# Optimization experiments

Measured on AMD Instinct MI355X. Metric: run time of the kernel, lower is better.

The kernel has to match this reference:

```python
import jax, jax.numpy as jnp
import numpy as np

N = 1_000_000      # occupied input voxels
NREF = 400_000     # occupied reference (target) voxels on the stride-2 grid
CIN = 32
COUT = 64
G = 256            # input spatial grid extent per axis
B = 4              # batch size (ME batch index in coords[:, 0])
PRIME = 2654435761 # odd -> bijective multiplier mod 2^26


def _decode_np(ids, g):
    z = ids % g; ids = ids // g
    y = ids % g; ids = ids // g
    x = ids % g; b = ids // g
    return np.stack([b, x, y, z], axis=1).astype(np.int32)


def setup_inputs() -> dict:
    key = jax.random.key(0)
    k1, k2, k3 = jax.random.split(key, 3)
    # unique input voxel coordinates on a B x G^3 grid (bijection mod 2^26)
    ids_in = (np.arange(N, dtype=np.int64) * PRIME) % (B * G ** 3)
    coords = _decode_np(ids_in, G)                      # [N,4] (b,x,y,z), unique
    # unique reference coordinates on the stride-2 output grid
    gh = G // 2
    ids_ref = (np.arange(NREF, dtype=np.int64) * PRIME) % (B * gh ** 3)
    ref = _decode_np(ids_ref, gh)
    ref[:, 1:] *= 2                                     # ME tensor-stride-2 coords
    feats = jax.random.normal(k1, (N, CIN), jnp.float32)
    W = jax.random.normal(k2, (8, CIN, COUT), jnp.float32) * (1.0 / np.sqrt(8 * CIN))
    b = jax.random.normal(k3, (COUT,), jnp.float32) * 0.01
    return {"feats": feats, "W": W, "b": b,
            "coords": jnp.asarray(coords), "ref_coords": jnp.asarray(ref)}


def _ravel(c, step):
    # faithful to get_target_by_sp_tensor: batch-major ravel of 4 columns
    return c[:, 3] + c[:, 2] * step + c[:, 1] * step * step + c[:, 0] * step * step * step


def reference(feats, W, b, coords, ref_coords):
    n = coords.shape[0]
    # --- hash table of input voxels (sorted keys + permuted features) ---
    in_key = ((coords[:, 0] * G + coords[:, 1]) * G + coords[:, 2]) * G + coords[:, 3]
    order = jnp.argsort(in_key)
    skeys = in_key[order]
    sfeats = feats[order]
    # --- output coordinates: stride-2 downsample (kernel=2, stride=2) ---
    p = coords.at[:, 1:].set((coords[:, 1:] // 2) * 2)
    pkey = ((p[:, 0] * G + p[:, 1]) * G + p[:, 2]) * G + p[:, 3]
    out_key = jnp.unique(pkey, size=n, fill_value=-1)   # sorted, padded with -1
    valid = out_key >= 0
    ok = jnp.where(valid, out_key, 0)
    oz = ok % G; r = ok // G
    oy = r % G; r = r // G
    ox = r % G; ob = r // G
    out_coords = jnp.where(valid[:, None], jnp.stack([ob, ox, oy, oz], axis=1), -1)
    # --- sparse conv: gather the 2x2x2 children of each output voxel ---
    acc = jnp.zeros((n, W.shape[2]), feats.dtype)
    offsets = [(dx, dy, dz) for dx in (0, 1) for dy in (0, 1) for dz in (0, 1)]
    for i, (dx, dy, dz) in enumerate(offsets):
        ckey = out_key + dx * G * G + dy * G + dz
        idx = jnp.clip(jnp.searchsorted(skeys, ckey), 0, n - 1)
        found = (skeys[idx] == ckey) & valid
        f = jnp.where(found[:, None], sfeats[idx], 0.0)
        acc = acc + f @ W[i]
    out_feats = jnp.where(valid[:, None], acc + b, 0.0)
    # --- pruning mask: ravel + isin, faithful to get_target_by_sp_tensor ---
    step = jnp.maximum(out_coords.max(), ref_coords.max()).astype(jnp.int32) + 1
    min_value = jnp.minimum(out_coords.min(), ref_coords.min())
    shift = jnp.where(min_value < 0, -min_value, 0)
    oc = out_coords.at[:, 1:].add(shift)
    rc = ref_coords.at[:, 1:].add(shift)
    out1d = _ravel(oc, step)
    ref1d = _ravel(rc, step)
    sref = jnp.sort(ref1d)
    j = jnp.clip(jnp.searchsorted(sref, out1d), 0, sref.shape[0] - 1)
    mask = (sref[j] == out1d) & valid
    out_feats = jnp.where(mask[:, None], out_feats, 0.0)
    return out_coords, out_feats, mask
```

## Files before the change

### kernel.cpp

```cpp
#include <hip/hip_runtime.h>

#define WORDS_P  (1u << 18)
#define NBLK2    1024

typedef float f4_native __attribute__((ext_vector_type(4)));

__device__ __forceinline__ unsigned k23_of(int b, int x, int y, int z) {
  return ((unsigned)b << 21) | ((unsigned)(x >> 1) << 14) |
         ((unsigned)(y >> 1) << 7) | (unsigned)(z >> 1);
}

__device__ __forceinline__ void fill_slice(f4_native* __restrict__ of, size_t lo,
                                           size_t hi, unsigned tid, unsigned nthr) {
  f4_native z = {0.f, 0.f, 0.f, 0.f};
  for (size_t i = lo + tid; i < hi; i += nthr)
    __builtin_nontemporal_store(z, &of[i]);
}

__global__ __launch_bounds__(256) void fill_ws(f4_native* __restrict__ wsz, size_t n4) {
  size_t stride = (size_t)gridDim.x * 256u;
  f4_native z = {0.f, 0.f, 0.f, 0.f};
  for (size_t i = (size_t)blockIdx.x * 256u + threadIdx.x; i < n4; i += stride)
    wsz[i] = z;
}

__global__ __launch_bounds__(256) void build_fill(const int4* __restrict__ coords, int n,
                                                  const int4* __restrict__ ref, int nref,
                                                  unsigned* __restrict__ parbm,
                                                  unsigned* __restrict__ refbm,
                                                  f4_native* __restrict__ ofm,
                                                  size_t lo, size_t hi) {
  unsigned tid = blockIdx.x * 256u + threadIdx.x;
  unsigned nthr = gridDim.x * 256u;
  for (unsigned i = tid; i < (unsigned)(n + nref); i += nthr) {
    if (i < (unsigned)n) {
      int4 c = coords[i];
      unsigned k = k23_of(c.x, c.y, c.z, c.w);
      atomicOr(&parbm[k >> 5], 1u << (k & 31));
    } else {
      int4 c = ref[i - (unsigned)n];
      unsigned k = k23_of(c.x, c.y, c.z, c.w);
      atomicOr(&refbm[k >> 5], 1u << (k & 31));
    }
  }
  fill_slice(ofm, lo, hi, tid, nthr);
}

__global__ __launch_bounds__(256) void pop2(const unsigned* __restrict__ parbm,
                                            unsigned* __restrict__ refbm,
                                            unsigned* __restrict__ bsums,
                                            f4_native* __restrict__ ofm,
                                            size_t lo, size_t hi) {
  __shared__ unsigned s[256];
  unsigned t = threadIdx.x;
  unsigned w = blockIdx.x * 256u + t;
  unsigned p = parbm[w];
  unsigned m = p & refbm[w];
  refbm[w] = m;
  s[t] = __popc(p); __syncthreads();
  for (int off = 128; off > 0; off >>= 1) { if (t < (unsigned)off) s[t] += s[t + off]; __syncthreads(); }
  if (t == 0) bsums[blockIdx.x] = s[0];
  __syncthreads();
  s[t] = __popc(m); __syncthreads();
  for (int off = 128; off > 0; off >>= 1) { if (t < (unsigned)off) s[t] += s[t + off]; __syncthreads(); }
  if (t == 0) bsums[NBLK2 + blockIdx.x] = s[0];

  fill_slice(ofm, lo, hi, blockIdx.x * 256u + t, gridDim.x * 256u);
}

__global__ __launch_bounds__(256) void prefix2b(const unsigned* __restrict__ parbm,
                                                const unsigned* __restrict__ maskbm,
                                                const unsigned* __restrict__ bsums,
                                                unsigned* __restrict__ parpre,
                                                unsigned* __restrict__ maskpre,
                                                unsigned* __restrict__ clist,
                                                unsigned* __restrict__ counter,
                                                f4_native* __restrict__ ofm,
                                                size_t lo, size_t hi) {
  __shared__ unsigned s[256];
  __shared__ unsigned basP_s, basM_s;
  unsigned t = threadIdx.x, blk = blockIdx.x;
  unsigned accP = 0, accM = 0;
  for (unsigned idx = t; idx < blk; idx += 256u) {
    accP += bsums[idx];
    accM += bsums[NBLK2 + idx];
  }
  s[t] = accP; __syncthreads();
  for (int off = 128; off > 0; off >>= 1) { if (t < (unsigned)off) s[t] += s[t + off]; __syncthreads(); }
  if (t == 0) basP_s = s[0];
  __syncthreads();
  s[t] = accM; __syncthreads();
  for (int off = 128; off > 0; off >>= 1) { if (t < (unsigned)off) s[t] += s[t + off]; __syncthreads(); }
  if (t == 0) basM_s = s[0];
  __syncthreads();
  unsigned basP = basP_s, basM = basM_s;

  unsigned w = blk * 256u + t;
  unsigned pw = parbm[w], mw = maskbm[w];
  unsigned cp = __popc(pw), cm = __popc(mw);
  s[t] = cp; __syncthreads();
  for (int off = 1; off < 256; off <<= 1) {
    unsigned v = (t >= (unsigned)off) ? s[t - off] : 0u;
    __syncthreads(); s[t] += v; __syncthreads();
  }
  unsigned ppre = basP + ((t == 0) ? 0u : s[t - 1]);
  parpre[w] = ppre;
  unsigned plast = basP + s[255];
  __syncthreads();
  s[t] = cm; __syncthreads();
  for (int off = 1; off < 256; off <<= 1) {
    unsigned v = (t >= (unsigned)off) ? s[t - off] : 0u;
    __syncthreads(); s[t] += v; __syncthreads();
  }
  unsigned mpre = basM + ((t == 0) ? 0u : s[t - 1]);
  maskpre[w] = mpre;
  for (unsigned k = 0; k < cm * 8u; k++) clist[mpre * 8u + k] = 0u;
  if (blk == NBLK2 - 1u && t == 255u) {
    counter[0] = basM + s[255];
    counter[1] = plast;
  }

  fill_slice(ofm, lo, hi, blk * 256u + t, gridDim.x * 256u);
}

__global__ __launch_bounds__(256) void scatter_emit(const int4* __restrict__ coords, int n,
                                                    const unsigned* __restrict__ parbm,
                                                    const unsigned* __restrict__ parpre,
                                                    const unsigned* __restrict__ maskbm,
                                                    const unsigned* __restrict__ maskpre,
                                                    const unsigned* __restrict__ counter,
                                                    unsigned* __restrict__ clist,
                                                    unsigned* __restrict__ mrow,
                                                    float4* __restrict__ out_coords,
                                                    float* __restrict__ out_mask,
                                                    f4_native* __restrict__ ofm,
                                                    size_t lo, size_t hi,
                                                    int nbN) {
  unsigned tid = blockIdx.x * 256u + threadIdx.x;
  unsigned nthr = gridDim.x * 256u;
  fill_slice(ofm, lo, hi, tid, nthr);

  if ((int)blockIdx.x < nbN) {
    int i = blockIdx.x * 256 + threadIdx.x;
    if (i >= n) return;
    int4 c = coords[i];
    unsigned k = k23_of(c.x, c.y, c.z, c.w);
    unsigned w = k >> 5, b = k & 31u;
    unsigned mw = maskbm[w];
    if ((mw >> b) & 1u) {
      unsigned j = maskpre[w] + __popc(mw & ((1u << b) - 1u));
      unsigned off = (((unsigned)c.y & 1u) << 2) | (((unsigned)c.z & 1u) << 1) |
                     ((unsigned)c.w & 1u);
      clist[j * 8u + off] = (unsigned)i + 1u;
    }
    return;
  }
  if ((int)blockIdx.x < nbN + (int)NBLK2) {
    unsigned w = (blockIdx.x - nbN) * 256u + threadIdx.x;
    unsigned bits = parbm[w];
    if (!bits) return;
    unsigned mb = maskbm[w];
    unsigned r = parpre[w];
    unsigned j = maskpre[w];
    while (bits) {
      unsigned b = (unsigned)__ffs((int)bits) - 1u;
      bits &= bits - 1u;
      unsigned k = (w << 5) | b;
      float bb = (float)(k >> 21);
      float x = (float)(((k >> 14) & 127u) << 1);
      float y = (float)(((k >> 7) & 127u) << 1);
      float z = (float)((k & 127u) << 1);
      out_coords[r] = make_float4(bb, x, y, z);
      if ((mb >> b) & 1u) {
        out_mask[r] = 1.0f;
        mrow[j++] = r;
      }
      r++;
    }
    return;
  }
  unsigned P = counter[1];
  unsigned idx = (blockIdx.x - nbN - NBLK2) * 256u + threadIdx.x;
  unsigned ntail = (unsigned)n - P;
  float4 m1 = make_float4(-1.f, -1.f, -1.f, -1.f);
  for (unsigned i = idx; i < ntail; i += 64u * 256u) out_coords[P + i] = m1;
}

__global__ __launch_bounds__(1024, 8) void conv_lds(const float* __restrict__ feats,
                                                    const float* __restrict__ Wg,
                                                    const float* __restrict__ bias,
                                                    const unsigned* __restrict__ clist,
                                                    const unsigned* __restrict__ mrow,
                                                    const unsigned* __restrict__ counter,
                                                    float* __restrict__ out_feats) {
  __shared__ float lw[16384];
  for (unsigned t = threadIdx.x; t < 4096u; t += 1024u)
    ((float4*)lw)[t] = ((const float4*)Wg)[t];
  __syncthreads();

  unsigned lane = threadIdx.x & 63u;
  unsigned wave = blockIdx.x * 16u + (threadIdx.x >> 6);
  unsigned nwaves = gridDim.x * 16u;
  unsigned M = counter[0];
  float bv = bias[lane];
  for (unsigned j = wave; j < M; j += nwaves) {
    unsigned r = mrow[j];
    uint4 c0 = *(const uint4*)(clist + (size_t)j * 8u);
    uint4 c1 = *(const uint4*)(clist + (size_t)j * 8u + 4u);
    unsigned cs[8] = {c0.x, c0.y, c0.z, c0.w, c1.x, c1.y, c1.z, c1.w};
    float acc = bv;
#pragma unroll
    for (int i = 0; i < 8; i++) {
      unsigned v = (unsigned)__builtin_amdgcn_readfirstlane((int)cs[i]);
      if (v) {
        const float* f = feats + (size_t)(v - 1u) * 32u;
        const float* wl = lw + i * 2048 + lane;
#pragma unroll
        for (int k = 0; k < 32; k++) acc = fmaf(f[k], wl[k * 64], acc);
      }
    }
    out_feats[(size_t)r * 64u + lane] = acc;
  }
}

extern "C" void kernel_launch(void* const* d_in, const int* in_sizes, int n_in,
                              void* d_out, int out_size, void* d_ws, size_t ws_size,
                              hipStream_t stream) {
  const float* feats = (const float*)d_in[0];
  const float* W     = (const float*)d_in[1];
  const float* bias  = (const float*)d_in[2];
  const int4*  coords = (const int4*)d_in[3];
  const int4*  ref    = (const int4*)d_in[4];
  int N    = in_sizes[0] / 32;
  int NREF = in_sizes[4] / 4;

  float* out_coords = (float*)d_out;
  float* out_feats  = out_coords + (size_t)N * 4;
  float* out_mask   = out_feats + (size_t)N * 64;

  char* ws = (char*)d_ws;
  unsigned* parbm   = (unsigned*)(ws);
  unsigned* refbm   = (unsigned*)(ws + (1u << 20));
  unsigned* maskbm  = refbm;
  unsigned* clist   = (unsigned*)(ws + (2u << 20));
  unsigned* parpre  = (unsigned*)(ws + (15u << 20));
  unsigned* maskpre = (unsigned*)(ws + (16u << 20));
  unsigned* mrow    = (unsigned*)(ws + (17u << 20));
  unsigned* bsums   = (unsigned*)(ws + (19u << 20));
  unsigned* counter = (unsigned*)(ws + (19u << 20) + 16384);

  int nbN = (N + 255) / 256;
  f4_native* ofm = (f4_native*)out_feats;
  size_t T  = (size_t)N * 65u / 4u;
  size_t T1 = T / 4, T2 = T / 2, T3 = 3 * (T / 4);

  fill_ws<<<64, 256, 0, stream>>>((f4_native*)ws, (size_t)(2u << 20) / 16u);
  build_fill<<<2048, 256, 0, stream>>>(coords, N, ref, NREF, parbm, refbm, ofm, T3, T);
  pop2<<<NBLK2, 256, 0, stream>>>(parbm, refbm, bsums, ofm, T2, T3);
  prefix2b<<<NBLK2, 256, 0, stream>>>(parbm, maskbm, bsums, parpre, maskpre, clist,
                                      counter, ofm, T1, T2);
  scatter_emit<<<nbN + NBLK2 + 64, 256, 0, stream>>>(coords, N, parbm, parpre, maskbm,
                                                     maskpre, counter, clist, mrow,
                                                     (float4*)out_coords, out_mask,
                                                     ofm, 0, T1, nbN);
  conv_lds<<<512, 1024, 0, stream>>>(feats, W, bias, clist, mrow, counter, out_feats);
}
```

Before: 132.8 us.

## Replace child-list gather conv with per-input atomic scatter conv

Drops the masked-row prefix scan, the clist/mrow child lists and their zeroing. The conv now walks the input voxels directly, finds each one's output row through the parent bitmap prefix and atomically adds its contribution into out_feats, which is pre-seeded with bias by the emit kernel. This removes one kernel launch and a scatter pass, and spreads the zero-fill over two kernels instead of four. In exchange it does up to 8 float atomics per output element and reads features in coordinate order rather than grouped by output row.

```diff
diff --git a/kernel.cpp b/kernel.cpp
--- a/kernel.cpp
+++ b/kernel.cpp
@@ -2,6 +2,7 @@
 
 #define WORDS_P  (1u << 18)
 #define NBLK2    1024
+#define CONVBLKS 512
 
 typedef float f4_native __attribute__((ext_vector_type(4)));
 
@@ -55,49 +56,39 @@
   unsigned t = threadIdx.x;
   unsigned w = blockIdx.x * 256u + t;
   unsigned p = parbm[w];
-  unsigned m = p & refbm[w];
-  refbm[w] = m;
+  refbm[w] = p & refbm[w];
   s[t] = __popc(p); __syncthreads();
   for (int off = 128; off > 0; off >>= 1) { if (t < (unsigned)off) s[t] += s[t + off]; __syncthreads(); }
   if (t == 0) bsums[blockIdx.x] = s[0];
-  __syncthreads();
-  s[t] = __popc(m); __syncthreads();
-  for (int off = 128; off > 0; off >>= 1) { if (t < (unsigned)off) s[t] += s[t + off]; __syncthreads(); }
-  if (t == 0) bsums[NBLK2 + blockIdx.x] = s[0];
 
   fill_slice(ofm, lo, hi, blockIdx.x * 256u + t, gridDim.x * 256u);
 }
 
-__global__ __launch_bounds__(256) void prefix2b(const unsigned* __restrict__ parbm,
-                                                const unsigned* __restrict__ maskbm,
-                                                const unsigned* __restrict__ bsums,
-                                                unsigned* __restrict__ parpre,
-                                                unsigned* __restrict__ maskpre,
-                                                unsigned* __restrict__ clist,
-                                                unsigned* __restrict__ counter,
-                                                f4_native* __restrict__ ofm,
-                                                size_t lo, size_t hi) {
+__global__ __launch_bounds__(256) void prefix_emit(const unsigned* __restrict__ parbm,
+                                                   const unsigned* __restrict__ maskbm,
+                                                   const unsigned* __restrict__ bsums,
+                                                   const float* __restrict__ bias,
+                                                   unsigned* __restrict__ parpre,
+                                                   unsigned* __restrict__ counter,
+                                                   float4* __restrict__ out_coords,
+                                                   float* __restrict__ out_mask,
+                                                   float* __restrict__ out_feats) {
   __shared__ unsigned s[256];
-  __shared__ unsigned basP_s, basM_s;
+  __shared__ unsigned basP_s;
+  __shared__ float4 lb4[16];
   unsigned t = threadIdx.x, blk = blockIdx.x;
-  unsigned accP = 0, accM = 0;
-  for (unsigned idx = t; idx < blk; idx += 256u) {
-    accP += bsums[idx];
-    accM += bsums[NBLK2 + idx];
-  }
+  if (t < 16u) lb4[t] = ((const float4*)bias)[t];
+  unsigned accP = 0;
+  for (unsigned idx = t; idx < blk; idx += 256u) accP += bsums[idx];
   s[t] = accP; __syncthreads();
   for (int off = 128; off > 0; off >>= 1) { if (t < (unsigned)off) s[t] += s[t + off]; __syncthreads(); }
   if (t == 0) basP_s = s[0];
   __syncthreads();
-  s[t] = accM; __syncthreads();
-  for (int off = 128; off > 0; off >>= 1) { if (t < (unsigned)off) s[t] += s[t + off]; __syncthreads(); }
-  if (t == 0) basM_s = s[0];
-  __syncthreads();
-  unsigned basP = basP_s, basM = basM_s;
+  unsigned basP = basP_s;
 
   unsigned w = blk * 256u + t;
   unsigned pw = parbm[w], mw = maskbm[w];
-  unsigned cp = __popc(pw), cm = __popc(mw);
+  unsigned cp = __popc(pw);
   s[t] = cp; __syncthreads();
   for (int off = 1; off < 256; off <<= 1) {
     unsigned v = (t >= (unsigned)off) ? s[t - off] : 0u;
@@ -105,94 +96,46 @@
   }
   unsigned ppre = basP + ((t == 0) ? 0u : s[t - 1]);
   parpre[w] = ppre;
-  unsigned plast = basP + s[255];
-  __syncthreads();
-  s[t] = cm; __syncthreads();
-  for (int off = 1; off < 256; off <<= 1) {
-    unsigned v = (t >= (unsigned)off) ? s[t - off] : 0u;
-    __syncthreads(); s[t] += v; __syncthreads();
-  }
-  unsigned mpre = basM + ((t == 0) ? 0u : s[t - 1]);
-  maskpre[w] = mpre;
-  for (unsigned k = 0; k < cm * 8u; k++) clist[mpre * 8u + k] = 0u;
-  if (blk == NBLK2 - 1u && t == 255u) {
-    counter[0] = basM + s[255];
-    counter[1] = plast;
-  }
-
-  fill_slice(ofm, lo, hi, blk * 256u + t, gridDim.x * 256u);
-}
-
-__global__ __launch_bounds__(256) void scatter_emit(const int4* __restrict__ coords, int n,
-                                                    const unsigned* __restrict__ parbm,
-                                                    const unsigned* __restrict__ parpre,
-                                                    const unsigned* __restrict__ maskbm,
-                                                    const unsigned* __restrict__ maskpre,
-                                                    const unsigned* __restrict__ counter,
-                                                    unsigned* __restrict__ clist,
-                                                    unsigned* __restrict__ mrow,
-                                                    float4* __restrict__ out_coords,
-                                                    float* __restrict__ out_mask,
-                                                    f4_native* __restrict__ ofm,
-                                                    size_t lo, size_t hi,
-                                                    int nbN) {
-  unsigned tid = blockIdx.x * 256u + threadIdx.x;
-  unsigned nthr = gridDim.x * 256u;
-  fill_slice(ofm, lo, hi, tid, nthr);
-
-  if ((int)blockIdx.x < nbN) {
-    int i = blockIdx.x * 256 + threadIdx.x;
-    if (i >= n) return;
-    int4 c = coords[i];
-    unsigned k = k23_of(c.x, c.y, c.z, c.w);
-    unsigned w = k >> 5, b = k & 31u;
-    unsigned mw = maskbm[w];
+  if (blk == NBLK2 - 1u && t == 255u) counter[1] = basP + s[255];
+
+  unsigned r = ppre, bits = pw;
+  while (bits) {
+    unsigned b = (unsigned)__ffs((int)bits) - 1u;
+    bits &= bits - 1u;
+    unsigned k = (w << 5) | b;
+    float bb = (float)(k >> 21);
+    float x = (float)(((k >> 14) & 127u) << 1);
+    float y = (float)(((k >> 7) & 127u) << 1);
+    float z = (float)((k & 127u) << 1);
+    out_coords[r] = make_float4(bb, x, y, z);
     if ((mw >> b) & 1u) {
-      unsigned j = maskpre[w] + __popc(mw & ((1u << b) - 1u));
-      unsigned off = (((unsigned)c.y & 1u) << 2) | (((unsigned)c.z & 1u) << 1) |
-                     ((unsigned)c.w & 1u);
-      clist[j * 8u + off] = (unsigned)i + 1u;
-    }
+      out_mask[r] = 1.0f;
+      float4* rp = (float4*)(out_feats + (size_t)r * 64u);
+#pragma unroll
+      for (int q = 0; q < 16; q++) rp[q] = lb4[q];
+    }
+    r++;
+  }
+}
+
+__global__ __launch_bounds__(1024, 8) void conv_scatter(const float* __restrict__ feats,
+                                                        const float* __restrict__ Wg,
+                                                        const int4* __restrict__ coords,
+                                                        const unsigned* __restrict__ parbm,
+                                                        const unsigned* __restrict__ parpre,
+                                                        const unsigned* __restrict__ maskbm,
+                                                        const unsigned* __restrict__ counter,
+                                                        int n,
+                                                        float* __restrict__ out_feats,
+                                                        float4* __restrict__ out_coords) {
+  if (blockIdx.x >= CONVBLKS) {
+    unsigned P = counter[1];
+    unsigned idx = (blockIdx.x - CONVBLKS) * 1024u + threadIdx.x;
+    unsigned ntail = (unsigned)n - P;
+    float4 m1 = make_float4(-1.f, -1.f, -1.f, -1.f);
+    for (unsigned i = idx; i < ntail; i += 64u * 1024u) out_coords[P + i] = m1;
     return;
   }
-  if ((int)blockIdx.x < nbN + (int)NBLK2) {
-    unsigned w = (blockIdx.x - nbN) * 256u + threadIdx.x;
-    unsigned bits = parbm[w];
-    if (!bits) return;
-    unsigned mb = maskbm[w];
-    unsigned r = parpre[w];
-    unsigned j = maskpre[w];
-    while (bits) {
-      unsigned b = (unsigned)__ffs((int)bits) - 1u;
-      bits &= bits - 1u;
-      unsigned k = (w << 5) | b;
-      float bb = (float)(k >> 21);
-      float x = (float)(((k >> 14) & 127u) << 1);
-      float y = (float)(((k >> 7) & 127u) << 1);
-      float z = (float)((k & 127u) << 1);
-      out_coords[r] = make_float4(bb, x, y, z);
-      if ((mb >> b) & 1u) {
-        out_mask[r] = 1.0f;
-        mrow[j++] = r;
-      }
-      r++;
-    }
-    return;
-  }
-  unsigned P = counter[1];
-  unsigned idx = (blockIdx.x - nbN - NBLK2) * 256u + threadIdx.x;
-  unsigned ntail = (unsigned)n - P;
-  float4 m1 = make_float4(-1.f, -1.f, -1.f, -1.f);
-  for (unsigned i = idx; i < ntail; i += 64u * 256u) out_coords[P + i] = m1;
-}
-
-__global__ __launch_bounds__(1024, 8) void conv_lds(const float* __restrict__ feats,
-                                                    const float* __restrict__ Wg,
-                                                    const float* __restrict__ bias,
-                                                    const unsigned* __restrict__ clist,
-                                                    const unsigned* __restrict__ mrow,
-                                                    const unsigned* __restrict__ counter,
-                                                    float* __restrict__ out_feats) {
   __shared__ float lw[16384];
   for (unsigned t = threadIdx.x; t < 4096u; t += 1024u)
     ((float4*)lw)[t] = ((const float4*)Wg)[t];
@@ -200,26 +143,38 @@
 
   unsigned lane = threadIdx.x & 63u;
   unsigned wave = blockIdx.x * 16u + (threadIdx.x >> 6);
-  unsigned nwaves = gridDim.x * 16u;
-  unsigned M = counter[0];
-  float bv = bias[lane];
-  for (unsigned j = wave; j < M; j += nwaves) {
-    unsigned r = mrow[j];
-    uint4 c0 = *(const uint4*)(clist + (size_t)j * 8u);
-    uint4 c1 = *(const uint4*)(clist + (size_t)j * 8u + 4u);
-    unsigned cs[8] = {c0.x, c0.y, c0.z, c0.w, c1.x, c1.y, c1.z, c1.w};
-    float acc = bv;
+  unsigned nwaves = CONVBLKS * 16u;
+  for (unsigned base = wave * 64u; base < (unsigned)n; base += nwaves * 64u) {
+    unsigned i = base + lane;
+    bool hit = false;
+    unsigned r = 0, off = 0;
+    if (i < (unsigned)n) {
+      int4 c = coords[i];
+      unsigned k = k23_of(c.x, c.y, c.z, c.w);
+      unsigned w = k >> 5, b = k & 31u;
+      unsigned mw = maskbm[w];
+      if ((mw >> b) & 1u) {
+        unsigned pw = parbm[w];
+        r = parpre[w] + __popc(pw & ((1u << b) - 1u));
+        off = (((unsigned)c.y & 1u) << 2) | (((unsigned)c.z & 1u) << 1) |
+              ((unsigned)c.w & 1u);
+        hit = true;
+      }
+    }
+    unsigned long long hm = __ballot(hit);
+    while (hm) {
+      int l = __ffsll((long long)hm) - 1;
+      hm &= hm - 1ull;
+      unsigned rr = (unsigned)__builtin_amdgcn_readfirstlane(__shfl((int)r, l, 64));
+      unsigned oo = (unsigned)__builtin_amdgcn_readfirstlane(__shfl((int)off, l, 64));
+      unsigned ii = (unsigned)__builtin_amdgcn_readfirstlane(__shfl((int)i, l, 64));
+      const float* f = feats + (size_t)ii * 32u;
+      const float* wl = lw + oo * 2048u + lane;
+      float acc = 0.f;
 #pragma unroll
-    for (int i = 0; i < 8; i++) {
-      unsigned v = (unsigned)__builtin_amdgcn_readfirstlane((int)cs[i]);
-      if (v) {
-        const float* f = feats + (size_t)(v - 1u) * 32u;
-        const float* wl = lw + i * 2048 + lane;
-#pragma unroll
-        for (int k = 0; k < 32; k++) acc = fmaf(f[k], wl[k * 64], acc);
-      }
-    }
-    out_feats[(size_t)r * 64u + lane] = acc;
+      for (int k = 0; k < 32; k++) acc = fmaf(f[k], wl[k * 64], acc);
+      atomicAdd(&out_feats[(size_t)rr * 64u + lane], acc);
+    }
   }
 }
 
@@ -242,26 +197,20 @@
   unsigned* parbm   = (unsigned*)(ws);
   unsigned* refbm   = (unsigned*)(ws + (1u << 20));
   unsigned* maskbm  = refbm;
-  unsigned* clist   = (unsigned*)(ws + (2u << 20));
-  unsigned* parpre  = (unsigned*)(ws + (15u << 20));
-  unsigned* maskpre = (unsigned*)(ws + (16u << 20));
-  unsigned* mrow    = (unsigned*)(ws + (17u << 20));
-  unsigned* bsums   = (unsigned*)(ws + (19u << 20));
-  unsigned* counter = (unsigned*)(ws + (19u << 20) + 16384);
-
-  int nbN = (N + 255) / 256;
+  unsigned* parpre  = (unsigned*)(ws + (2u << 20));
+  unsigned* bsums   = (unsigned*)(ws + (3u << 20));
+  unsigned* counter = (unsigned*)(ws + (3u << 20) + 8192);
+
   f4_native* ofm = (f4_native*)out_feats;
   size_t T  = (size_t)N * 65u / 4u;
-  size_t T1 = T / 4, T2 = T / 2, T3 = 3 * (T / 4);
-
-  fill_ws<<<64, 256, 0, stream>>>((f4_native*)ws, (size_t)(2u << 20) / 16u);
-  build_fill<<<2048, 256, 0, stream>>>(coords, N, ref, NREF, parbm, refbm, ofm, T3, T);
-  pop2<<<NBLK2, 256, 0, stream>>>(parbm, refbm, bsums, ofm, T2, T3);
-  prefix2b<<<NBLK2, 256, 0, stream>>>(parbm, maskbm, bsums, parpre, maskpre, clist,
-                                      counter, ofm, T1, T2);
-  scatter_emit<<<nbN + NBLK2 + 64, 256, 0, stream>>>(coords, N, parbm, parpre, maskbm,
-                                                     maskpre, counter, clist, mrow,
-                                                     (float4*)out_coords, out_mask,
-                                                     ofm, 0, T1, nbN);
-  conv_lds<<<512, 1024, 0, stream>>>(feats, W, bias, clist, mrow, counter, out_feats);
-}
+  size_t Th = T / 2;
+
+  fill_ws<<<64, 256, 0, stream>>>((f4_native*)ws, ((size_t)(2u << 20) + 8192u + 16u) / 16u);
+  build_fill<<<2048, 256, 0, stream>>>(coords, N, ref, NREF, parbm, refbm, ofm, Th, T);
+  pop2<<<NBLK2, 256, 0, stream>>>(parbm, refbm, bsums, ofm, 0, Th);
+  prefix_emit<<<NBLK2, 256, 0, stream>>>(parbm, maskbm, bsums, bias, parpre, counter,
+                                         (float4*)out_coords, out_mask, out_feats);
+  conv_scatter<<<CONVBLKS + 64, 1024, 0, stream>>>(feats, W, coords, parbm, parpre,
+                                                   maskbm, counter, N, out_feats,
+                                                   (float4*)out_coords);
+}
```

Result: slower. 137.9 us (+3.8%).
